# Optimization experiments

Measured on AMD Instinct MI355X. Metric: run time of the kernel, lower is better.

The kernel has to match this reference:

```python
import jax, jax.numpy as jnp
import numpy as np

N = 100000   # nodes
E = 1600000  # directed edges (avg degree 16)
IN = 256     # input feature dim


def _gcn_norm(src, dst, n):
    # PyG gcn_norm with unit edge weights: deg computed on destination,
    # norm = deg^{-1/2}[src] * deg^{-1/2}[dst]
    deg = jax.ops.segment_sum(jnp.ones_like(dst, jnp.float32), dst, num_segments=n)
    dinv = jnp.where(deg > 0, jax.lax.rsqrt(deg), 0.0)
    return dinv[src] * dinv[dst]


def _gcn_conv(x, W, b, src, dst, norm, n):
    h = x @ W                          # [N, out] dense transform first (PyG order)
    msg = norm[:, None] * h[src]       # gather + scale  [E+N, out]
    agg = jax.ops.segment_sum(msg, dst, num_segments=n)  # scatter-add
    return agg + b


def setup_inputs() -> dict:
    key = jax.random.key(0)
    ks = jax.random.split(key, 5)
    x = jax.random.normal(ks[0], (N, IN), jnp.float32)
    edge_index = jax.random.randint(ks[1], (2, E), 0, N, dtype=jnp.int32)
    W1 = jax.random.normal(ks[2], (IN, 64), jnp.float32) * (1.0 / np.sqrt(IN))
    b1 = jnp.zeros((64,), jnp.float32)
    W2 = jax.random.normal(ks[3], (64, 32), jnp.float32) * (1.0 / np.sqrt(64))
    b2 = jnp.zeros((32,), jnp.float32)
    Wlin = jax.random.normal(ks[4], (32, 1), jnp.float32) * (1.0 / np.sqrt(32))
    blin = jnp.zeros((1,), jnp.float32)
    return {"x": x, "edge_index": edge_index, "W1": W1, "b1": b1,
            "W2": W2, "b2": b2, "Wlin": Wlin, "blin": blin}


def reference(x, edge_index, W1, b1, W2, b2, Wlin, blin):
    n = x.shape[0]
    loops = jnp.arange(n, dtype=edge_index.dtype)  # add self-loops (GCNConv default)
    src = jnp.concatenate([edge_index[0], loops])
    dst = jnp.concatenate([edge_index[1], loops])
    norm = _gcn_norm(src, dst, n)                  # same for both layers
    h = jax.nn.relu(_gcn_conv(x, W1, b1, src, dst, norm, n))
    h = jax.nn.relu(_gcn_conv(h, W2, b2, src, dst, norm, n))
    return h @ Wlin + blin
```

## Files before the change

### kernel.cpp

```cpp
#include <hip/hip_runtime.h>
#include <hip/hip_fp16.h>
#include <math.h>


#define BSH  9
#define BCAP 12288

typedef _Float16 half8 __attribute__((ext_vector_type(8)));
typedef float floatx4 __attribute__((ext_vector_type(4)));

static __global__ __launch_bounds__(256) void k_wfrag(const float* __restrict__ W1,
                                                      _Float16* __restrict__ w1f) {
    int t = threadIdx.x;
    for (int idx = t; idx < 2048; idx += 256) {
        int kb = idx >> 8;
        int nt = (idx >> 6) & 3;
        int l  = idx & 63;
        int k0 = kb * 32 + ((l >> 4) << 3);
        int nn = nt * 16 + (l & 15);
        half8 b;
        #pragma unroll
        for (int j = 0; j < 8; ++j) b[j] = (_Float16)W1[(k0 + j) * 64 + nn];
        *(half8*)(w1f + (size_t)idx * 8) = b;
    }
}

static __global__ __launch_bounds__(256, 4) void k_fat(const float* __restrict__ x,
                                                       const _Float16* __restrict__ w1f,
                                                       _Float16* __restrict__ h1f,
                                                       const int* __restrict__ src,
                                                       const int* __restrict__ dst,
                                                       int* __restrict__ bkt_cnt,
                                                       int* __restrict__ epack,
                                                       int n, int e, int nScat) {
    __shared__ alignas(16) char smem[32768];
    int t = threadIdx.x;

    if ((int)blockIdx.x < nScat) {
        int*           sp    = (int*)smem;
        unsigned char* sbkt  = (unsigned char*)(smem + 16384);
        int*           cnt   = (int*)(smem + 20480);
        int*           loff  = (int*)(smem + 21504);
        int*           lcur  = (int*)(smem + 22528);
        int*           gbase = (int*)(smem + 23552);
        int*           sh    = (int*)(smem + 24576);
        int cb = blockIdx.x * 4096;
        int cc = min(4096, e - cb);

        cnt[t] = 0;
        __syncthreads();
        int ep[16]; unsigned char eb[16];
        int nv = 0;
        #pragma unroll
        for (int k = 0; k < 16; ++k) {
            int i = cb + k * 256 + t;
            if (i < e) {
                int s = src[i], d = dst[i];
                int b = d >> BSH;
                ep[nv] = ((d & 511) << 17) | s;
                eb[nv] = (unsigned char)b;
                atomicAdd(&cnt[b], 1);
                ++nv;
            }
        }
        __syncthreads();
        int v = cnt[t];
        sh[t] = v;
        __syncthreads();
        for (int o = 1; o < 256; o <<= 1) {
            int u = (t >= o) ? sh[t - o] : 0;
            __syncthreads();
            sh[t] += u;
            __syncthreads();
        }
        loff[t] = sh[t] - v;
        lcur[t] = sh[t] - v;
        if (v > 0) gbase[t] = t * BCAP + atomicAdd(&bkt_cnt[t], v);
        __syncthreads();
        for (int k = 0; k < nv; ++k) {
            int b = eb[k];
            int p = atomicAdd(&lcur[b], 1);
            sp[p] = ep[k];
            sbkt[p] = (unsigned char)b;
        }
        __syncthreads();
        for (int i = t; i < cc; i += 256) {
            int b = sbkt[i];
            epack[gbase[b] + (i - loff[b])] = sp[i];
        }
    } else {
        _Float16* Wl = (_Float16*)smem;
        {
            const float4* s = (const float4*)w1f;
            float4* d = (float4*)smem;
            #pragma unroll
            for (int i = 0; i < 8; ++i) d[t + i * 256] = s[t + i * 256];
        }
        __syncthreads();

        int l = t & 63;
        int w = t >> 6;
        int r0 = (blockIdx.x - nScat) * 128 + w * 32;
        int kq = (l >> 4) << 3;
        int ra0 = r0 + (l & 15);
        int ra1 = ra0 + 16;
        ra0 = ra0 < n ? ra0 : n - 1;
        ra1 = ra1 < n ? ra1 : n - 1;
        const float* p0 = x + (size_t)ra0 * 256 + kq;
        const float* p1 = x + (size_t)ra1 * 256 + kq;

        floatx4 acc[2][4];
        #pragma unroll
        for (int mt = 0; mt < 2; ++mt)
            #pragma unroll
            for (int nt = 0; nt < 4; ++nt)
                acc[mt][nt] = (floatx4){0.f, 0.f, 0.f, 0.f};

        float4 cu0 = *(const float4*)(p0);
        float4 cu1 = *(const float4*)(p0 + 4);
        float4 cv0 = *(const float4*)(p1);
        float4 cv1 = *(const float4*)(p1 + 4);

        #pragma unroll
        for (int kb = 0; kb < 8; ++kb) {
            float4 nu0, nu1, nv0, nv1;
            if (kb < 7) {
                nu0 = *(const float4*)(p0 + (kb + 1) * 32);
                nu1 = *(const float4*)(p0 + (kb + 1) * 32 + 4);
                nv0 = *(const float4*)(p1 + (kb + 1) * 32);
                nv1 = *(const float4*)(p1 + (kb + 1) * 32 + 4);
            }
            half8 a0, a1;
            a0[0] = (_Float16)cu0.x; a0[1] = (_Float16)cu0.y; a0[2] = (_Float16)cu0.z; a0[3] = (_Float16)cu0.w;
            a0[4] = (_Float16)cu1.x; a0[5] = (_Float16)cu1.y; a0[6] = (_Float16)cu1.z; a0[7] = (_Float16)cu1.w;
            a1[0] = (_Float16)cv0.x; a1[1] = (_Float16)cv0.y; a1[2] = (_Float16)cv0.z; a1[3] = (_Float16)cv0.w;
            a1[4] = (_Float16)cv1.x; a1[5] = (_Float16)cv1.y; a1[6] = (_Float16)cv1.z; a1[7] = (_Float16)cv1.w;
            #pragma unroll
            for (int nt = 0; nt < 4; ++nt) {
                half8 b = *(const half8*)(Wl + ((size_t)(kb * 4 + nt) * 64 + l) * 8);
                acc[0][nt] = __builtin_amdgcn_mfma_f32_16x16x32_f16(a0, b, acc[0][nt], 0, 0, 0);
                acc[1][nt] = __builtin_amdgcn_mfma_f32_16x16x32_f16(a1, b, acc[1][nt], 0, 0, 0);
            }
            cu0 = nu0; cu1 = nu1; cv0 = nv0; cv1 = nv1;
        }

        int quad = l >> 4;
        int col  = l & 15;
        #pragma unroll
        for (int mt = 0; mt < 2; ++mt) {
            #pragma unroll
            for (int r = 0; r < 4; ++r) {
                int rr = r0 + mt * 16 + quad * 4 + r;
                if (rr < n) {
                    _Float16* o = h1f + (size_t)rr * 64 + col;
                    #pragma unroll
                    for (int nt = 0; nt < 4; ++nt)
                        o[nt * 16] = (_Float16)acc[mt][nt][r];
                }
            }
        }
    }
}

static __global__ __launch_bounds__(512) void k_bfinal(const int* __restrict__ bkt_cnt,
                                                       const int* __restrict__ epack,
                                                       float* __restrict__ dinv,
                                                       int* __restrict__ offs,
                                                       int* __restrict__ csr_src, int n) {
    __shared__ int cnt[512], sh[512], lcur[512];
    int t = threadIdx.x;
    int base = blockIdx.x << BSH;
    int e0 = blockIdx.x * BCAP;
    int e1 = e0 + bkt_cnt[blockIdx.x];
    cnt[t] = 0;
    __syncthreads();
    for (int i = e0 + t; i < e1; i += 512) atomicAdd(&cnt[epack[i] >> 17], 1);
    __syncthreads();
    int v = cnt[t];
    if (base + t < n) dinv[base + t] = 1.0f / sqrtf((float)(v + 1));
    sh[t] = v;
    __syncthreads();
    for (int o = 1; o < 512; o <<= 1) {
        int u = (t >= o) ? sh[t - o] : 0;
        __syncthreads();
        sh[t] += u;
        __syncthreads();
    }
    int incl = sh[t];
    if (base + t < n) offs[base + t] = e0 + incl;
    lcur[t] = e0 + incl - v;
    __syncthreads();
    for (int i = e0 + t; i < e1; i += 512) {
        int p = epack[i];
        int d = p >> 17;
        int pos = atomicAdd(&lcur[d], 1);
        csr_src[pos] = p & 0x1FFFF;
    }
}

static __global__ __launch_bounds__(512) void k_wpack(int* __restrict__ csr_src,
                                                      const float* __restrict__ dinv,
                                                      const int* __restrict__ bkt_cnt) {
    int b  = blockIdx.x;
    int e0 = b * BCAP;
    int e1 = e0 + bkt_cnt[b];
    for (int i = e0 + threadIdx.x; i < e1; i += 512) {
        int s = csr_src[i];
        int q = (int)(dinv[s] * 32767.0f + 0.5f);
        csr_src[i] = s | (q << 17);
    }
}

static __global__ __launch_bounds__(256) void k_agg1gemm2(const int* __restrict__ offs,
                                                          const int* __restrict__ csr_src,
                                                          const float* __restrict__ dinv,
                                                          const __half2* __restrict__ h1h,
                                                          const float* __restrict__ b1,
                                                          const float* __restrict__ W2,
                                                          __half* __restrict__ h2h, int n) {
    __shared__ float Wl[64 * 32];
    __shared__ float aggL[8][64];
    int t = threadIdx.x;
    *(float4*)(Wl + t * 4)        = *(const float4*)(W2 + t * 4);
    *(float4*)(Wl + t * 4 + 1024) = *(const float4*)(W2 + t * 4 + 1024);

    int li = t & 31;
    int ni = t >> 5;
    int node  = blockIdx.x * 8 + ni;
    int nodeC = node < n ? node : n - 1;
    int start = (nodeC & 511) ? offs[nodeC - 1] : (nodeC >> BSH) * BCAP;
    int end   = offs[nodeC];
    float dd  = dinv[nodeC];
    float2 hf = __half22float2(h1h[(size_t)nodeC * 32 + li]);
    float accx = dd * hf.x, accy = dd * hf.y;

    const float QS = 1.0f / 32767.0f;
    int j = start;
    for (; j + 7 < end; j += 8) {
        int pk[8];
        #pragma unroll
        for (int u = 0; u < 8; ++u) pk[u] = csr_src[j + u];
        float2 vv[8]; float wq[8];
        #pragma unroll
        for (int u = 0; u < 8; ++u) {
            int s = pk[u] & 0x1FFFF;
            wq[u] = (float)(((unsigned)pk[u]) >> 17) * QS;
            vv[u] = __half22float2(h1h[(size_t)s * 32 + li]);
        }
        #pragma unroll
        for (int u = 0; u < 8; ++u) { accx += wq[u] * vv[u].x; accy += wq[u] * vv[u].y; }
    }
    for (; j < end; ++j) {
        int p = csr_src[j];
        int s = p & 0x1FFFF;
        float w = (float)(((unsigned)p) >> 17) * QS;
        float2 v = __half22float2(h1h[(size_t)s * 32 + li]);
        accx += w * v.x;
        accy += w * v.y;
    }
    float2 bb = ((const float2*)b1)[li];
    aggL[ni][2 * li + 0] = fmaxf(dd * accx + bb.x, 0.f);
    aggL[ni][2 * li + 1] = fmaxf(dd * accy + bb.y, 0.f);
    __syncthreads();

    if (node < n) {
        float s = 0.f;
        #pragma unroll
        for (int k = 0; k < 64; ++k) s += aggL[ni][k] * Wl[k * 32 + li];
        h2h[(size_t)node * 32 + li] = __float2half(s);
    }
}

static __global__ __launch_bounds__(256) void k_gather2f(const int* __restrict__ offs,
                                                         const int* __restrict__ csr_src,
                                                         const float* __restrict__ dinv,
                                                         const __half2* __restrict__ h2h,
                                                         const float* __restrict__ b2,
                                                         const float* __restrict__ Wlin,
                                                         const float* __restrict__ blin,
                                                         float* __restrict__ out, int n) {
    int g    = blockIdx.x * 256 + threadIdx.x;
    int node = g >> 4;
    if (node >= n) return;
    int li = g & 15;
    int start = (node & 511) ? offs[node - 1] : (node >> BSH) * BCAP;
    int end   = offs[node];
    float dd  = dinv[node];
    float2 hf = __half22float2(h2h[(size_t)node * 16 + li]);
    float accx = dd * hf.x, accy = dd * hf.y;

    const float QS = 1.0f / 32767.0f;
    int j = start;
    for (; j + 7 < end; j += 8) {
        int pk[8];
        #pragma unroll
        for (int u = 0; u < 8; ++u) pk[u] = csr_src[j + u];
        float2 vv[8]; float wq[8];
        #pragma unroll
        for (int u = 0; u < 8; ++u) {
            int s = pk[u] & 0x1FFFF;
            wq[u] = (float)(((unsigned)pk[u]) >> 17) * QS;
            vv[u] = __half22float2(h2h[(size_t)s * 16 + li]);
        }
        #pragma unroll
        for (int u = 0; u < 8; ++u) { accx += wq[u] * vv[u].x; accy += wq[u] * vv[u].y; }
    }
    for (; j < end; ++j) {
        int p = csr_src[j];
        int s = p & 0x1FFFF;
        float w = (float)(((unsigned)p) >> 17) * QS;
        float2 v = __half22float2(h2h[(size_t)s * 16 + li]);
        accx += w * v.x;
        accy += w * v.y;
    }
    float2 bb = ((const float2*)b2)[li];
    float2 wl = ((const float2*)Wlin)[li];
    float val = fmaxf(dd * accx + bb.x, 0.f) * wl.x +
                fmaxf(dd * accy + bb.y, 0.f) * wl.y;
    #pragma unroll
    for (int m = 8; m >= 1; m >>= 1) val += __shfl_xor(val, m);
    if (li == 0) out[node] = val + blin[0];
}

extern "C" void kernel_launch(void* const* d_in, const int* in_sizes, int n_in,
                              void* d_out, int out_size, void* d_ws, size_t ws_size,
                              hipStream_t stream) {
    const float* x    = (const float*)d_in[0];
    const int*   ei   = (const int*)d_in[1];
    const float* W1   = (const float*)d_in[2];
    const float* b1   = (const float*)d_in[3];
    const float* W2   = (const float*)d_in[4];
    const float* b2   = (const float*)d_in[5];
    const float* Wlin = (const float*)d_in[6];
    const float* blin = (const float*)d_in[7];
    float* out = (float*)d_out;

    const int n = in_sizes[0] / 256;
    const int e = in_sizes[1] / 2;
    const int* src = ei;
    const int* dst = ei + e;
    const int nbkt  = (n + (1 << BSH) - 1) >> BSH;
    const int nScat = (e + 4095) / 4096;
    const int nGemm = (n + 127) / 128;

    char* wp = (char*)d_ws;
    __half2*  h1h = (__half2*)wp;
    _Float16* h1f = (_Float16*)wp;    wp += (size_t)n * 32 * 4;
    __half*   h2h = (__half*)wp;      wp += (size_t)n * 32 * 2;
    float*    dinv = (float*)wp;      wp += (size_t)n * 4;
    int*      offs = (int*)wp;        wp += (size_t)n * 4;
    int*      csr_src = (int*)wp;     wp += (size_t)nbkt * BCAP * 4;
    int*      epack = (int*)wp;       wp += (size_t)nbkt * BCAP * 4;
    int*      bkt_cnt = (int*)wp;     wp += 256 * 4;
    _Float16* w1f = (_Float16*)wp;

    dim3 B(256);
    hipMemsetAsync(bkt_cnt, 0, 256 * 4, stream);
    k_wfrag <<<1, B, 0, stream>>>(W1, w1f);
    k_fat   <<<nScat + nGemm, B, 0, stream>>>(x, w1f, h1f, src, dst, bkt_cnt, epack, n, e, nScat);
    k_bfinal<<<nbkt, 512, 0, stream>>>(bkt_cnt, epack, dinv, offs, csr_src, n);
    k_wpack <<<nbkt, 512, 0, stream>>>(csr_src, dinv, bkt_cnt);
    k_agg1gemm2<<<(n + 7) / 8, B, 0, stream>>>(offs, csr_src, dinv, h1h, b1, W2, h2h, n);
    k_gather2f <<<(n * 16 + 255) / 256, B, 0, stream>>>(offs, csr_src, dinv, (const __half2*)h2h,
                                                        b2, Wlin, blin, out, n);
}
```

Before: 304.2 us.

## Widen gathers to 8-byte loads, stage x tiles in LDS, fold memset

The two aggregation kernels now have each lane gather 4 halfs (uint2) per neighbour instead of 2. That halves lanes per node, doubles nodes per block, and gives wider and fewer memory requests. The layer-1 GEMM now loads coalesced x tiles into padded LDS once per k-block instead of doing per-lane strided register prefetch. This adds two barriers per k-step and drops the occupancy hint. The bucket-count memset is folded into the weight-fragment kernel to remove one API call.

```diff
diff --git a/kernel.cpp b/kernel.cpp
--- a/kernel.cpp
+++ b/kernel.cpp
@@ -7,11 +7,16 @@
 #define BCAP 12288
 
 typedef _Float16 half8 __attribute__((ext_vector_type(8)));
+typedef _Float16 half4 __attribute__((ext_vector_type(4)));
 typedef float floatx4 __attribute__((ext_vector_type(4)));
 
+#define XT_STRIDE 40
+
 static __global__ __launch_bounds__(256) void k_wfrag(const float* __restrict__ W1,
-                                                      _Float16* __restrict__ w1f) {
+                                                      _Float16* __restrict__ w1f,
+                                                      int* __restrict__ bkt_cnt) {
     int t = threadIdx.x;
+    bkt_cnt[t] = 0;
     for (int idx = t; idx < 2048; idx += 256) {
         int kb = idx >> 8;
         int nt = (idx >> 6) & 3;
@@ -25,15 +30,15 @@
     }
 }
 
-static __global__ __launch_bounds__(256, 4) void k_fat(const float* __restrict__ x,
-                                                       const _Float16* __restrict__ w1f,
-                                                       _Float16* __restrict__ h1f,
-                                                       const int* __restrict__ src,
-                                                       const int* __restrict__ dst,
-                                                       int* __restrict__ bkt_cnt,
-                                                       int* __restrict__ epack,
-                                                       int n, int e, int nScat) {
-    __shared__ alignas(16) char smem[32768];
+static __global__ __launch_bounds__(256) void k_fat(const float* __restrict__ x,
+                                                    const _Float16* __restrict__ w1f,
+                                                    _Float16* __restrict__ h1f,
+                                                    const int* __restrict__ src,
+                                                    const int* __restrict__ dst,
+                                                    int* __restrict__ bkt_cnt,
+                                                    int* __restrict__ epack,
+                                                    int n, int e, int nScat) {
+    __shared__ alignas(16) char smem[32768 + 128 * XT_STRIDE * 2];
     int t = threadIdx.x;
 
     if ((int)blockIdx.x < nScat) {
@@ -90,24 +95,20 @@
         }
     } else {
         _Float16* Wl = (_Float16*)smem;
+        _Float16* xt = (_Float16*)(smem + 32768);
         {
             const float4* s = (const float4*)w1f;
             float4* d = (float4*)smem;
             #pragma unroll
             for (int i = 0; i < 8; ++i) d[t + i * 256] = s[t + i * 256];
         }
-        __syncthreads();
 
         int l = t & 63;
         int w = t >> 6;
-        int r0 = (blockIdx.x - nScat) * 128 + w * 32;
+        int r0 = (blockIdx.x - nScat) * 128;
         int kq = (l >> 4) << 3;
-        int ra0 = r0 + (l & 15);
-        int ra1 = ra0 + 16;
-        ra0 = ra0 < n ? ra0 : n - 1;
-        ra1 = ra1 < n ? ra1 : n - 1;
-        const float* p0 = x + (size_t)ra0 * 256 + kq;
-        const float* p1 = x + (size_t)ra1 * 256 + kq;
+        int lrow0 = w * 32 + (l & 15);
+        int lrow1 = lrow0 + 16;
 
         floatx4 acc[2][4];
         #pragma unroll
@@ -116,41 +117,42 @@
             for (int nt = 0; nt < 4; ++nt)
                 acc[mt][nt] = (floatx4){0.f, 0.f, 0.f, 0.f};
 
-        float4 cu0 = *(const float4*)(p0);
-        float4 cu1 = *(const float4*)(p0 + 4);
-        float4 cv0 = *(const float4*)(p1);
-        float4 cv1 = *(const float4*)(p1 + 4);
-
         #pragma unroll
         for (int kb = 0; kb < 8; ++kb) {
-            float4 nu0, nu1, nv0, nv1;
-            if (kb < 7) {
-                nu0 = *(const float4*)(p0 + (kb + 1) * 32);
-                nu1 = *(const float4*)(p0 + (kb + 1) * 32 + 4);
-                nv0 = *(const float4*)(p1 + (kb + 1) * 32);
-                nv1 = *(const float4*)(p1 + (kb + 1) * 32 + 4);
+            __syncthreads();
+            #pragma unroll
+            for (int i = 0; i < 4; ++i) {
+                int f   = t + i * 256;
+                int row = f >> 3;
+                int c4  = f & 7;
+                int gr  = r0 + row;
+                gr = gr < n ? gr : n - 1;
+                float4 v = *(const float4*)(x + (size_t)gr * 256 + kb * 32 + c4 * 4);
+                half4 h;
+                h[0] = (_Float16)v.x; h[1] = (_Float16)v.y;
+                h[2] = (_Float16)v.z; h[3] = (_Float16)v.w;
+                *(half4*)(xt + row * XT_STRIDE + c4 * 4) = h;
             }
-            half8 a0, a1;
-            a0[0] = (_Float16)cu0.x; a0[1] = (_Float16)cu0.y; a0[2] = (_Float16)cu0.z; a0[3] = (_Float16)cu0.w;
-            a0[4] = (_Float16)cu1.x; a0[5] = (_Float16)cu1.y; a0[6] = (_Float16)cu1.z; a0[7] = (_Float16)cu1.w;
-            a1[0] = (_Float16)cv0.x; a1[1] = (_Float16)cv0.y; a1[2] = (_Float16)cv0.z; a1[3] = (_Float16)cv0.w;
-            a1[4] = (_Float16)cv1.x; a1[5] = (_Float16)cv1.y; a1[6] = (_Float16)cv1.z; a1[7] = (_Float16)cv1.w;
+            __syncthreads();
+
+            half8 a0 = *(const half8*)(xt + lrow0 * XT_STRIDE + kq);
+            half8 a1 = *(const half8*)(xt + lrow1 * XT_STRIDE + kq);
             #pragma unroll
             for (int nt = 0; nt < 4; ++nt) {
                 half8 b = *(const half8*)(Wl + ((size_t)(kb * 4 + nt) * 64 + l) * 8);
                 acc[0][nt] = __builtin_amdgcn_mfma_f32_16x16x32_f16(a0, b, acc[0][nt], 0, 0, 0);
                 acc[1][nt] = __builtin_amdgcn_mfma_f32_16x16x32_f16(a1, b, acc[1][nt], 0, 0, 0);
             }
-            cu0 = nu0; cu1 = nu1; cv0 = nv0; cv1 = nv1;
         }
 
         int quad = l >> 4;
         int col  = l & 15;
+        int rb0  = r0 + w * 32;
         #pragma unroll
         for (int mt = 0; mt < 2; ++mt) {
             #pragma unroll
             for (int r = 0; r < 4; ++r) {
-                int rr = r0 + mt * 16 + quad * 4 + r;
+                int rr = rb0 + mt * 16 + quad * 4 + r;
                 if (rr < n) {
                     _Float16* o = h1f + (size_t)rr * 64 + col;
                     #pragma unroll
@@ -214,25 +216,28 @@
 static __global__ __launch_bounds__(256) void k_agg1gemm2(const int* __restrict__ offs,
                                                           const int* __restrict__ csr_src,
                                                           const float* __restrict__ dinv,
-                                                          const __half2* __restrict__ h1h,
+                                                          const uint2* __restrict__ h1q,
                                                           const float* __restrict__ b1,
                                                           const float* __restrict__ W2,
-                                                          __half* __restrict__ h2h, int n) {
+                                                          __half2* __restrict__ h2h, int n) {
     __shared__ float Wl[64 * 32];
-    __shared__ float aggL[8][64];
+    __shared__ float aggL[16][64];
     int t = threadIdx.x;
     *(float4*)(Wl + t * 4)        = *(const float4*)(W2 + t * 4);
     *(float4*)(Wl + t * 4 + 1024) = *(const float4*)(W2 + t * 4 + 1024);
 
-    int li = t & 31;
-    int ni = t >> 5;
-    int node  = blockIdx.x * 8 + ni;
+    int li = t & 15;
+    int ni = t >> 4;
+    int node  = blockIdx.x * 16 + ni;
     int nodeC = node < n ? node : n - 1;
     int start = (nodeC & 511) ? offs[nodeC - 1] : (nodeC >> BSH) * BCAP;
     int end   = offs[nodeC];
     float dd  = dinv[nodeC];
-    float2 hf = __half22float2(h1h[(size_t)nodeC * 32 + li]);
-    float accx = dd * hf.x, accy = dd * hf.y;
+
+    uint2 su = h1q[(size_t)nodeC * 16 + li];
+    float2 s01 = __half22float2(*(const __half2*)&su.x);
+    float2 s23 = __half22float2(*(const __half2*)&su.y);
+    float a0 = dd * s01.x, a1 = dd * s01.y, a2 = dd * s23.x, a3 = dd * s23.y;
 
     const float QS = 1.0f / 32767.0f;
     int j = start;
@@ -240,54 +245,71 @@
         int pk[8];
         #pragma unroll
         for (int u = 0; u < 8; ++u) pk[u] = csr_src[j + u];
-        float2 vv[8]; float wq[8];
+        uint2 vv[8]; float wq[8];
         #pragma unroll
         for (int u = 0; u < 8; ++u) {
             int s = pk[u] & 0x1FFFF;
             wq[u] = (float)(((unsigned)pk[u]) >> 17) * QS;
-            vv[u] = __half22float2(h1h[(size_t)s * 32 + li]);
-        }
-        #pragma unroll
-        for (int u = 0; u < 8; ++u) { accx += wq[u] * vv[u].x; accy += wq[u] * vv[u].y; }
+            vv[u] = h1q[(size_t)s * 16 + li];
+        }
+        #pragma unroll
+        for (int u = 0; u < 8; ++u) {
+            float2 v01 = __half22float2(*(const __half2*)&vv[u].x);
+            float2 v23 = __half22float2(*(const __half2*)&vv[u].y);
+            a0 += wq[u] * v01.x; a1 += wq[u] * v01.y;
+            a2 += wq[u] * v23.x; a3 += wq[u] * v23.y;
+        }
     }
     for (; j < end; ++j) {
         int p = csr_src[j];
         int s = p & 0x1FFFF;
-        float w = (float)(((unsigned)p) >> 17) * QS;
-        float2 v = __half22float2(h1h[(size_t)s * 32 + li]);
-        accx += w * v.x;
-        accy += w * v.y;
-    }
-    float2 bb = ((const float2*)b1)[li];
-    aggL[ni][2 * li + 0] = fmaxf(dd * accx + bb.x, 0.f);
-    aggL[ni][2 * li + 1] = fmaxf(dd * accy + bb.y, 0.f);
+        float wv = (float)(((unsigned)p) >> 17) * QS;
+        uint2 v = h1q[(size_t)s * 16 + li];
+        float2 v01 = __half22float2(*(const __half2*)&v.x);
+        float2 v23 = __half22float2(*(const __half2*)&v.y);
+        a0 += wv * v01.x; a1 += wv * v01.y;
+        a2 += wv * v23.x; a3 += wv * v23.y;
+    }
+    float4 bb = *(const float4*)(b1 + li * 4);
+    aggL[ni][li * 4 + 0] = fmaxf(dd * a0 + bb.x, 0.f);
+    aggL[ni][li * 4 + 1] = fmaxf(dd * a1 + bb.y, 0.f);
+    aggL[ni][li * 4 + 2] = fmaxf(dd * a2 + bb.z, 0.f);
+    aggL[ni][li * 4 + 3] = fmaxf(dd * a3 + bb.w, 0.f);
     __syncthreads();
 
     if (node < n) {
-        float s = 0.f;
-        #pragma unroll
-        for (int k = 0; k < 64; ++k) s += aggL[ni][k] * Wl[k * 32 + li];
-        h2h[(size_t)node * 32 + li] = __float2half(s);
+        float s0 = 0.f, s1 = 0.f;
+        #pragma unroll
+        for (int k = 0; k < 64; ++k) {
+            float a = aggL[ni][k];
+            float2 wv = *(const float2*)(Wl + k * 32 + li * 2);
+            s0 += a * wv.x;
+            s1 += a * wv.y;
+        }
+        h2h[(size_t)node * 16 + li] = __float22half2_rn(make_float2(s0, s1));
     }
 }
 
 static __global__ __launch_bounds__(256) void k_gather2f(const int* __restrict__ offs,
                                                          const int* __restrict__ csr_src,
                                                          const float* __restrict__ dinv,
-                                                         const __half2* __restrict__ h2h,
+                                                         const uint2* __restrict__ h2q,
                                                          const float* __restrict__ b2,
                                                          const float* __restrict__ Wlin,
                                                          const float* __restrict__ blin,
                                                          float* __restrict__ out, int n) {
     int g    = blockIdx.x * 256 + threadIdx.x;
-    int node = g >> 4;
+    int node = g >> 3;
     if (node >= n) return;
-    int li = g & 15;
+    int li = g & 7;
     int start = (node & 511) ? offs[node - 1] : (node >> BSH) * BCAP;
     int end   = offs[node];
     float dd  = dinv[node];
-    float2 hf = __half22float2(h2h[(size_t)node * 16 + li]);
-    float accx = dd * hf.x, accy = dd * hf.y;
+
+    uint2 su = h2q[(size_t)node * 8 + li];
+    float2 s01 = __half22float2(*(const __half2*)&su.x);
+    float2 s23 = __half22float2(*(const __half2*)&su.y);
+    float a0 = dd * s01.x, a1 = dd * s01.y, a2 = dd * s23.x, a3 = dd * s23.y;
 
     const float QS = 1.0f / 32767.0f;
     int j = start;
@@ -295,30 +317,40 @@
         int pk[8];
         #pragma unroll
         for (int u = 0; u < 8; ++u) pk[u] = csr_src[j + u];
-        float2 vv[8]; float wq[8];
+        uint2 vv[8]; float wq[8];
         #pragma unroll
         for (int u = 0; u < 8; ++u) {
             int s = pk[u] & 0x1FFFF;
             wq[u] = (float)(((unsigned)pk[u]) >> 17) * QS;
-            vv[u] = __half22float2(h2h[(size_t)s * 16 + li]);
-        }
-        #pragma unroll
-        for (int u = 0; u < 8; ++u) { accx += wq[u] * vv[u].x; accy += wq[u] * vv[u].y; }
+            vv[u] = h2q[(size_t)s * 8 + li];
+        }
+        #pragma unroll
+        for (int u = 0; u < 8; ++u) {
+            float2 v01 = __half22float2(*(const __half2*)&vv[u].x);
+            float2 v23 = __half22float2(*(const __half2*)&vv[u].y);
+            a0 += wq[u] * v01.x; a1 += wq[u] * v01.y;
+            a2 += wq[u] * v23.x; a3 += wq[u] * v23.y;
+        }
     }
     for (; j < end; ++j) {
         int p = csr_src[j];
         int s = p & 0x1FFFF;
-        float w = (float)(((unsigned)p) >> 17) * QS;
-        float2 v = __half22float2(h2h[(size_t)s * 16 + li]);
-        accx += w * v.x;
-        accy += w * v.y;
-    }
-    float2 bb = ((const float2*)b2)[li];
-    float2 wl = ((const float2*)Wlin)[li];
-    float val = fmaxf(dd * accx + bb.x, 0.f) * wl.x +
-                fmaxf(dd * accy + bb.y, 0.f) * wl.y;
-    #pragma unroll
-    for (int m = 8; m >= 1; m >>= 1) val += __shfl_xor(val, m);
+        float wv = (float)(((unsigned)p) >> 17) * QS;
+        uint2 v = h2q[(size_t)s * 8 + li];
+        float2 v01 = __half22float2(*(const __half2*)&v.x);
+        float2 v23 = __half22float2(*(const __half2*)&v.y);
+        a0 += wv * v01.x; a1 += wv * v01.y;
+        a2 += wv * v23.x; a3 += wv * v23.y;
+    }
+    float4 bb = *(const float4*)(b2 + li * 4);
+    float4 wl = *(const float4*)(Wlin + li * 4);
+    float val = fmaxf(dd * a0 + bb.x, 0.f) * wl.x +
+                fmaxf(dd * a1 + bb.y, 0.f) * wl.y +
+                fmaxf(dd * a2 + bb.z, 0.f) * wl.z +
+                fmaxf(dd * a3 + bb.w, 0.f) * wl.w;
+    val += __shfl_xor(val, 4);
+    val += __shfl_xor(val, 2);
+    val += __shfl_xor(val, 1);
     if (li == 0) out[node] = val + blin[0];
 }
 
@@ -344,9 +376,10 @@
     const int nGemm = (n + 127) / 128;
 
     char* wp = (char*)d_ws;
-    __half2*  h1h = (__half2*)wp;
-    _Float16* h1f = (_Float16*)wp;    wp += (size_t)n * 32 * 4;
-    __half*   h2h = (__half*)wp;      wp += (size_t)n * 32 * 2;
+    _Float16* h1f = (_Float16*)wp;
+    uint2*    h1q = (uint2*)wp;       wp += (size_t)n * 32 * 4;
+    __half2*  h2h = (__half2*)wp;
+    uint2*    h2q = (uint2*)wp;       wp += (size_t)n * 32 * 2;
     float*    dinv = (float*)wp;      wp += (size_t)n * 4;
     int*      offs = (int*)wp;        wp += (size_t)n * 4;
     int*      csr_src = (int*)wp;     wp += (size_t)nbkt * BCAP * 4;
@@ -355,12 +388,11 @@
     _Float16* w1f = (_Float16*)wp;
 
     dim3 B(256);
-    hipMemsetAsync(bkt_cnt, 0, 256 * 4, stream);
-    k_wfrag <<<1, B, 0, stream>>>(W1, w1f);
+    k_wfrag <<<1, B, 0, stream>>>(W1, w1f, bkt_cnt);
     k_fat   <<<nScat + nGemm, B, 0, stream>>>(x, w1f, h1f, src, dst, bkt_cnt, epack, n, e, nScat);
     k_bfinal<<<nbkt, 512, 0, stream>>>(bkt_cnt, epack, dinv, offs, csr_src, n);
     k_wpack <<<nbkt, 512, 0, stream>>>(csr_src, dinv, bkt_cnt);
-    k_agg1gemm2<<<(n + 7) / 8, B, 0, stream>>>(offs, csr_src, dinv, h1h, b1, W2, h2h, n);
-    k_gather2f <<<(n * 16 + 255) / 256, B, 0, stream>>>(offs, csr_src, dinv, (const __half2*)h2h,
-                                                        b2, Wlin, blin, out, n);
-}
+    k_agg1gemm2<<<(n + 15) / 16, B, 0, stream>>>(offs, csr_src, dinv, h1q, b1, W2, h2h, n);
+    k_gather2f <<<(n * 8 + 255) / 256, B, 0, stream>>>(offs, csr_src, dinv, h2q,
+                                                       b2, Wlin, blin, out, n);
+}
```

After: 291.3 us. -4.2%, faster.
